# Kernel optimization log

Hardware: AMD Instinct MI355X
Metric: run time of the kernel (lower is better)

## Reference

```python
import jax, jax.numpy as jnp
import numpy as np

EMBED_DIM = 1024
NUM_HEADS = 16
HEAD_DIM = EMBED_DIM // NUM_HEADS
B, S = 4, 4096


def maxpool1d_2(x):
    # MaxPooling1D(pool_size=2, strides=2, padding='same'); seq len is even so no padding needed.
    n, l, d = x.shape
    return jnp.max(x.reshape(n, l // 2, 2, d), axis=2)


def setup_inputs() -> dict:
    key = jax.random.key(0)
    ks = jax.random.split(key, 5)
    scale = 1.0 / np.sqrt(EMBED_DIM)
    return {
        "x": jax.random.normal(ks[0], (B, S, EMBED_DIM), dtype=jnp.float32),
        "Wq": jax.random.normal(ks[1], (EMBED_DIM, EMBED_DIM), dtype=jnp.float32) * scale,
        "bq": jnp.zeros((EMBED_DIM,), dtype=jnp.float32),
        "Wk": jax.random.normal(ks[2], (EMBED_DIM, EMBED_DIM), dtype=jnp.float32) * scale,
        "bk": jnp.zeros((EMBED_DIM,), dtype=jnp.float32),
        "Wv": jax.random.normal(ks[3], (EMBED_DIM, EMBED_DIM), dtype=jnp.float32) * scale,
        "bv": jnp.zeros((EMBED_DIM,), dtype=jnp.float32),
        "Wo": jax.random.normal(ks[4], (EMBED_DIM, EMBED_DIM), dtype=jnp.float32) * scale,
        "bo": jnp.zeros((EMBED_DIM,), dtype=jnp.float32),
    }


def _separate_heads_pool(x, batch_size):
    # [B, S, E] -> [B, S, H, hd] -> [B, H, S, hd] -> [B*H, S, hd] -> pooled [B*H, S/2, hd]
    n, s, _ = x.shape
    x = x.reshape(batch_size, s, NUM_HEADS, HEAD_DIM).transpose(0, 2, 1, 3)
    x = x.reshape(batch_size * NUM_HEADS, s, HEAD_DIM)
    return maxpool1d_2(x)


def reference(x, Wq, bq, Wk, bk, Wv, bv, Wo, bo):
    batch_size = x.shape[0]
    q = x @ Wq + bq
    k = x @ Wk + bk
    v = x @ Wv + bv
    q = _separate_heads_pool(q, batch_size)  # [B*H, S/2, hd]
    k = _separate_heads_pool(k, batch_size)
    v = _separate_heads_pool(v, batch_size)
    score = jnp.einsum('nqd,nkd->nqk', q, k) / jnp.sqrt(jnp.float32(HEAD_DIM))
    weights = jax.nn.softmax(score, axis=-1)
    attn = jnp.einsum('nqk,nkd->nqd', weights, v)  # [B*H, S/2, hd]
    attn = maxpool1d_2(attn)  # [B*H, S/4, hd]
    # reshape back: (batch, -1, head_dim*num_heads). NOTE: original reshapes
    # [B*H, S/4, hd] directly to (B, -1, E) without transposing heads back,
    # so we replicate that exact layout.
    attn = attn.reshape(batch_size, -1, HEAD_DIM * NUM_HEADS)  # [B, S/4 (head-major mix), E]
    return attn @ Wo + bo
```

## Files before the change

### kernel.cpp

```cpp
#include <hip/hip_runtime.h>
#include <stdint.h>

typedef __attribute__((ext_vector_type(8))) __bf16 bf16x8;
typedef __attribute__((ext_vector_type(4))) float f32x4;
typedef __attribute__((ext_vector_type(8))) int i32x8;

#define DEV __device__ __forceinline__

DEV unsigned short f2bf(float f) {
  union { float f; uint32_t u; } v; v.f = f;
  return (unsigned short)((v.u + 0x7fffu + ((v.u >> 16) & 1u)) >> 16);
}

DEV uint32_t pk2bf(float lo, float hi) {
  union { float f; uint32_t u; } a, b;
  a.f = lo; b.f = hi;
  return __builtin_amdgcn_perm(b.u + 0x8000u, a.u + 0x8000u, 0x07060302u);
}

DEV void gld16(const void* g, void* l) {
  __builtin_amdgcn_global_load_lds(
      (const __attribute__((address_space(1))) uint32_t*)g,
      (__attribute__((address_space(3))) uint32_t*)l, 16, 0, 0);
}

union Frag8 { i32x8 v; uint4 q[2]; };

__global__ __launch_bounds__(256) void k_cvt_x(const float* __restrict__ x,
                                               uint8_t* __restrict__ x8) {
  size_t t = (size_t)blockIdx.x * 256 + threadIdx.x;
  const float4* xv = (const float4*)x;
  float4 a = xv[t * 2], b = xv[t * 2 + 1];
  int lo = 0, hi = 0;
  lo = __builtin_amdgcn_cvt_pk_fp8_f32(a.x, a.y, lo, false);
  lo = __builtin_amdgcn_cvt_pk_fp8_f32(a.z, a.w, lo, true);
  hi = __builtin_amdgcn_cvt_pk_fp8_f32(b.x, b.y, hi, false);
  hi = __builtin_amdgcn_cvt_pk_fp8_f32(b.z, b.w, hi, true);
  int2 pk; pk.x = lo; pk.y = hi;
  *(int2*)&x8[t * 8] = pk;
}

__global__ void k_cvt_w(const float* __restrict__ W0, const float* __restrict__ W1,
                        const float* __restrict__ W2, const float* __restrict__ W3,
                        uint8_t* __restrict__ W8, unsigned short* __restrict__ WoT) {
  const int z = blockIdx.z;
  const float* W = (z == 0) ? W0 : (z == 1) ? W1 : (z == 2) ? W2 : W3;
  __shared__ float tile[32][33];
  const int n0 = blockIdx.x * 32, k0 = blockIdx.y * 32;
  const int tx = threadIdx.x, ty = threadIdx.y;
  const int tid = ty * 32 + tx;
#pragma unroll
  for (int i = 0; i < 4; i++)
    tile[ty * 4 + i][tx] = W[(size_t)(k0 + ty * 4 + i) * 1024 + n0 + tx];
  __syncthreads();
  if (z < 3) {
    int nn = tid >> 3, kg = tid & 7;
    int w_ = 0;
    w_ = __builtin_amdgcn_cvt_pk_fp8_f32(32.f * tile[kg * 4 + 0][nn],
                                         32.f * tile[kg * 4 + 1][nn], w_, false);
    w_ = __builtin_amdgcn_cvt_pk_fp8_f32(32.f * tile[kg * 4 + 2][nn],
                                         32.f * tile[kg * 4 + 3][nn], w_, true);
    *(uint32_t*)&W8[(size_t)z * 1048576 + (size_t)(n0 + nn) * 1024 + k0 + kg * 4] =
        (uint32_t)w_;
  } else {
#pragma unroll
    for (int i = 0; i < 4; i++)
      WoT[(size_t)(n0 + ty * 4 + i) * 1024 + k0 + tx] = f2bf(tile[tx][ty * 4 + i]);
  }
}

__global__ __launch_bounds__(256) void k_gemm_qkv(
    const uint8_t* __restrict__ A, const uint8_t* __restrict__ W8,
    const float* __restrict__ bq, const float* __restrict__ bk,
    const float* __restrict__ bv,
    unsigned short* __restrict__ Qp, unsigned short* __restrict__ Kp,
    unsigned short* __restrict__ Vt) {
  const int tid = threadIdx.x;
  int flat = (blockIdx.z * 128 + blockIdx.y) * 8 + blockIdx.x;
  int swz = (flat & 7) * 384 + (flat >> 3);
  const int n0 = (swz & 7) * 128;
  const int m0 = ((swz >> 3) & 127) * 128;
  const int z = swz >> 10;
  const uint8_t* Bt = W8 + (size_t)z * 1048576;
  const float* bias = (z == 0) ? bq : (z == 1) ? bk : bv;

  __shared__ __align__(16) uint8_t lA[128 * 128];
  __shared__ __align__(16) uint8_t lB[128 * 128];

  const int lane = tid & 63, w = tid >> 6;
  const int wr = w >> 1, wc = w & 1;
  const int r = lane & 15, qd = lane >> 4;
  const int rl = lane >> 3, sg = lane & 7;

  f32x4 acc[4][4];
#pragma unroll
  for (int i = 0; i < 4; i++)
#pragma unroll
    for (int j = 0; j < 4; j++) acc[i][j] = (f32x4){0.f, 0.f, 0.f, 0.f};

  for (int k0 = 0; k0 < 1024; k0 += 128) {
    __syncthreads();
#pragma unroll
    for (int p = 0; p < 4; p++) {
      int row = (p * 4 + w) * 8 + rl;
      int g = sg ^ (row & 7);
      gld16(&A[(size_t)(m0 + row) * 1024 + k0 + g * 16], &lA[row * 128 + sg * 16]);
      gld16(&Bt[(size_t)(n0 + row) * 1024 + k0 + g * 16], &lB[row * 128 + sg * 16]);
    }
    __syncthreads();
    Frag8 bfr[4];
#pragma unroll
    for (int nt = 0; nt < 4; nt++) {
      int row = wc * 64 + nt * 16 + r;
      int g0 = (2 * qd) ^ (row & 7), g1 = (2 * qd + 1) ^ (row & 7);
      bfr[nt].q[0] = *(const uint4*)&lB[row * 128 + g0 * 16];
      bfr[nt].q[1] = *(const uint4*)&lB[row * 128 + g1 * 16];
    }
#pragma unroll
    for (int mt = 0; mt < 4; mt++) {
      int row = wr * 64 + mt * 16 + r;
      int g0 = (2 * qd) ^ (row & 7), g1 = (2 * qd + 1) ^ (row & 7);
      Frag8 af;
      af.q[0] = *(const uint4*)&lA[row * 128 + g0 * 16];
      af.q[1] = *(const uint4*)&lA[row * 128 + g1 * 16];
#pragma unroll
      for (int nt = 0; nt < 4; nt++)
        acc[mt][nt] = __builtin_amdgcn_mfma_scale_f32_16x16x128_f8f6f4(
            af.v, bfr[nt].v, acc[mt][nt], 0, 0, 0, 0x7f7f7f7f, 0, 0x7f7f7f7f);
    }
  }

  unsigned short* OP = (z == 0) ? Qp : Kp;
#pragma unroll
  for (int nt = 0; nt < 4; nt++) {
    int n = n0 + wc * 64 + nt * 16 + r;
    float bv_ = bias[n];
    int h = n >> 6, d = n & 63;
#pragma unroll
    for (int mt = 0; mt < 4; mt++) {
      int mg = m0 + wr * 64 + mt * 16 + qd * 4;
      int b = mg >> 12, s2 = (mg & 4095) >> 1;
      int bh = b * 16 + h;
      f32x4 a = acc[mt][nt];
      float v0 = fmaxf(a.x, a.y) * 0.03125f + bv_;
      float v1 = fmaxf(a.z, a.w) * 0.03125f + bv_;
      if (z == 2) {
        uint32_t pk = (uint32_t)f2bf(v0) | ((uint32_t)f2bf(v1) << 16);
        *(uint32_t*)&Vt[((size_t)bh * 64 + d) * 2048 + s2] = pk;
      } else {
        size_t base = ((size_t)bh * 2048 + s2) * 64 + d;
        OP[base] = f2bf(v0);
        OP[base + 64] = f2bf(v1);
      }
    }
  }
}

__global__ __launch_bounds__(256) void k_gemm_out(
    const unsigned short* __restrict__ A, const unsigned short* __restrict__ Bt,
    const float* __restrict__ bias, float* __restrict__ fout) {
  const int tid = threadIdx.x;
  int flat = blockIdx.y * 8 + blockIdx.x;
  int swz = (flat & 7) * 32 + (flat >> 3);
  const int n0 = (swz & 7) * 128, m0 = (swz >> 3) * 128;

  __shared__ __align__(16) unsigned short lA[128 * 64];
  __shared__ __align__(16) unsigned short lB[128 * 64];

  const int lane = tid & 63, w = tid >> 6;
  const int wr = w >> 1, wc = w & 1;
  const int r = lane & 15, qd = lane >> 4;
  const int srow = tid >> 3, sg = tid & 7;

  f32x4 acc[4][4];
#pragma unroll
  for (int i = 0; i < 4; i++)
#pragma unroll
    for (int j = 0; j < 4; j++) acc[i][j] = (f32x4){0.f, 0.f, 0.f, 0.f};

  for (int k0 = 0; k0 < 1024; k0 += 64) {
    __syncthreads();
#pragma unroll
    for (int p = 0; p < 4; p++) {
      int row = p * 32 + srow;
      int gs = sg ^ (row & 7);
      gld16(&A[(size_t)(m0 + row) * 1024 + k0 + gs * 8], &lA[row * 64 + sg * 8]);
      gld16(&Bt[(size_t)(n0 + row) * 1024 + k0 + gs * 8], &lB[row * 64 + sg * 8]);
    }
    __syncthreads();
#pragma unroll
    for (int kf = 0; kf < 2; kf++) {
      bf16x8 af[4], bfr[4];
#pragma unroll
      for (int mt = 0; mt < 4; mt++) {
        int row = wr * 64 + mt * 16 + r;
        int lg = (kf * 4 + qd) ^ (row & 7);
        af[mt] = *(const bf16x8*)&lA[row * 64 + lg * 8];
      }
#pragma unroll
      for (int nt = 0; nt < 4; nt++) {
        int row = wc * 64 + nt * 16 + r;
        int lg = (kf * 4 + qd) ^ (row & 7);
        bfr[nt] = *(const bf16x8*)&lB[row * 64 + lg * 8];
      }
#pragma unroll
      for (int mt = 0; mt < 4; mt++)
#pragma unroll
        for (int nt = 0; nt < 4; nt++)
          acc[mt][nt] = __builtin_amdgcn_mfma_f32_16x16x32_bf16(af[mt], bfr[nt],
                                                               acc[mt][nt], 0, 0, 0);
    }
  }

#pragma unroll
  for (int nt = 0; nt < 4; nt++) {
    int n = n0 + wc * 64 + nt * 16 + r;
    float bv = bias[n];
#pragma unroll
    for (int mt = 0; mt < 4; mt++) {
      int mg = m0 + wr * 64 + mt * 16 + qd * 4;
      f32x4 a = acc[mt][nt];
      fout[(size_t)(mg + 0) * 1024 + n] = a.x + bv;
      fout[(size_t)(mg + 1) * 1024 + n] = a.y + bv;
      fout[(size_t)(mg + 2) * 1024 + n] = a.z + bv;
      fout[(size_t)(mg + 3) * 1024 + n] = a.w + bv;
    }
  }
}

__global__ __launch_bounds__(256) void k_attn(const unsigned short* __restrict__ Qp,
                                              const unsigned short* __restrict__ Kp,
                                              const unsigned short* __restrict__ Vt,
                                              unsigned short* __restrict__ Am) {
  const int tid = threadIdx.x;
  int flat = blockIdx.y * 32 + blockIdx.x;
  int swz = (flat & 7) * 256 + (flat >> 3);
  const int qt = swz & 31, bh = swz >> 5;
  const int w = tid >> 6, lane = tid & 63;
  const int r = lane & 15, qd = lane >> 4;
  const int srow = tid >> 3, sg = tid & 7;

  __shared__ __align__(16) unsigned short lK[64 * 64];
  __shared__ __align__(16) unsigned short lV[64 * 64];
  __shared__ __align__(16) unsigned short lP[4][16 * 80];

  const int q0 = qt * 64;
  const int qrow = q0 + w * 16 + r;
  const size_t qbase = ((size_t)bh * 2048 + qrow) * 64;
  const bf16x8 bq0 = *(const bf16x8*)&Qp[qbase + qd * 8];
  const bf16x8 bq1 = *(const bf16x8*)&Qp[qbase + 32 + qd * 8];

  const unsigned short* Kg = Kp + (size_t)bh * 2048 * 64;
  const unsigned short* Vg = Vt + (size_t)bh * 64 * 2048;

  const float K2 = 0.125f * 1.44269504f;

  float lsum = 0.f;
  f32x4 accO[4];
#pragma unroll
  for (int i = 0; i < 4; i++) accO[i] = (f32x4){0.f, 0.f, 0.f, 0.f};

  char* lPw = (char*)&lP[w][0];

  for (int kb = 0; kb < 2048; kb += 64) {
    __syncthreads();
#pragma unroll
    for (int c = 0; c < 2; c++) {
      int row = c * 32 + srow;
      int gs = sg ^ (row & 7);
      gld16(&Kg[(size_t)(kb + row) * 64 + gs * 8], &lK[row * 64 + sg * 8]);
      gld16(&Vg[(size_t)row * 2048 + kb + gs * 8], &lV[row * 64 + sg * 8]);
    }
    __syncthreads();

    f32x4 s[4];
#pragma unroll
    for (int mt = 0; mt < 4; mt++) {
      int row = mt * 16 + r;
      int lg0 = qd ^ (row & 7), lg1 = (4 + qd) ^ (row & 7);
      bf16x8 ak0 = *(const bf16x8*)&lK[row * 64 + lg0 * 8];
      bf16x8 ak1 = *(const bf16x8*)&lK[row * 64 + lg1 * 8];
      s[mt] = (f32x4){0.f, 0.f, 0.f, 0.f};
      s[mt] = __builtin_amdgcn_mfma_f32_16x16x32_bf16(ak0, bq0, s[mt], 0, 0, 0);
      s[mt] = __builtin_amdgcn_mfma_f32_16x16x32_bf16(ak1, bq1, s[mt], 0, 0, 0);
    }

#pragma unroll
    for (int mt = 0; mt < 4; mt++) {
      float p0 = __builtin_amdgcn_exp2f(fmaf(s[mt][0], K2, -0.5f));
      float p1 = __builtin_amdgcn_exp2f(fmaf(s[mt][1], K2, -0.5f));
      float p2 = __builtin_amdgcn_exp2f(fmaf(s[mt][2], K2, -0.5f));
      float p3 = __builtin_amdgcn_exp2f(fmaf(s[mt][3], K2, -0.5f));
      lsum += (p0 + p1) + (p2 + p3);
      uint2 dw; dw.x = pk2bf(p0, p1); dw.y = pk2bf(p2, p3);
      int off = r * 160 + (((2 * mt + (qd >> 1)) ^ (r & 7)) << 4) + ((qd & 1) << 3);
      *(uint2*)(lPw + off) = dw;
    }

    bf16x8 ap0 = *(const bf16x8*)(lPw + r * 160 + ((qd ^ (r & 7)) << 4));
    bf16x8 ap1 = *(const bf16x8*)(lPw + r * 160 + (((4 + qd) ^ (r & 7)) << 4));

#pragma unroll
    for (int nt = 0; nt < 4; nt++) {
      int row = nt * 16 + r;
      int lg0 = qd ^ (row & 7), lg1 = (4 + qd) ^ (row & 7);
      bf16x8 bv0 = *(const bf16x8*)&lV[row * 64 + lg0 * 8];
      bf16x8 bv1 = *(const bf16x8*)&lV[row * 64 + lg1 * 8];
      accO[nt] = __builtin_amdgcn_mfma_f32_16x16x32_bf16(ap0, bv0, accO[nt], 0, 0, 0);
      accO[nt] = __builtin_amdgcn_mfma_f32_16x16x32_bf16(ap1, bv1, accO[nt], 0, 0, 0);
    }
  }

  lsum += __shfl_xor(lsum, 16, 64);
  lsum += __shfl_xor(lsum, 32, 64);
  float linv = 1.f / lsum;
  float inv[4];
#pragma unroll
  for (int g = 0; g < 4; g++) inv[g] = __shfl(linv, qd * 4 + g, 64);

#pragma unroll
  for (int nt = 0; nt < 4; nt++) {
    int d = nt * 16 + r;
    int s4 = (q0 + w * 16 + qd * 4) >> 1;
    float o0 = fmaxf(accO[nt][0] * inv[0], accO[nt][1] * inv[1]);
    float o1 = fmaxf(accO[nt][2] * inv[2], accO[nt][3] * inv[3]);
    size_t base = ((size_t)bh * 1024 + s4) * 64 + d;
    Am[base] = f2bf(o0);
    Am[base + 64] = f2bf(o1);
  }
}

extern "C" void kernel_launch(void* const* d_in, const int* in_sizes, int n_in,
                              void* d_out, int out_size, void* d_ws, size_t ws_size,
                              hipStream_t stream) {
  const float* x  = (const float*)d_in[0];
  const float* Wq = (const float*)d_in[1];
  const float* bq = (const float*)d_in[2];
  const float* Wk = (const float*)d_in[3];
  const float* bk = (const float*)d_in[4];
  const float* Wv = (const float*)d_in[5];
  const float* bv = (const float*)d_in[6];
  const float* Wo = (const float*)d_in[7];
  const float* bo = (const float*)d_in[8];
  float* out = (float*)d_out;

  uint8_t* ws = (uint8_t*)d_ws;
  uint8_t*        x8  = ws;
  uint8_t*        W8  = ws + 16777216;
  unsigned short* WoT = (unsigned short*)(ws + 19922944);
  unsigned short* Qp  = (unsigned short*)(ws + 22020096);
  unsigned short* Kp  = (unsigned short*)(ws + 38797312);
  unsigned short* Vt  = (unsigned short*)(ws + 55574528);
  unsigned short* Am  = (unsigned short*)(ws + 72351744);

  k_cvt_x<<<8192, 256, 0, stream>>>(x, x8);
  k_cvt_w<<<dim3(32, 32, 4), dim3(32, 8), 0, stream>>>(Wq, Wk, Wv, Wo, W8, WoT);
  k_gemm_qkv<<<dim3(8, 128, 3), 256, 0, stream>>>(x8, W8, bq, bk, bv, Qp, Kp, Vt);
  k_attn<<<dim3(32, 64), 256, 0, stream>>>(Qp, Kp, Vt, Am);
  k_gemm_out<<<dim3(8, 32), 256, 0, stream>>>(Am, WoT, bo, out);
}
```

Baseline: 360.0 us.

## Double-buffer LDS tiles in QKV GEMM, output GEMM, and attention kernels

Converts the shared-memory staging in all three kernels to two ping-pong buffers. The next K-slice (or K/V block) is issued via global_load_lds before the current buffer is consumed, and one barrier per iteration replaces two. The aim is to hide global-to-LDS load latency behind MFMA work. In exchange LDS use per block doubles, which may lower occupancy, and correctness depends on the compiler's waitcnt handling before the barrier.

```diff
diff --git a/kernel.cpp b/kernel.cpp
--- a/kernel.cpp
+++ b/kernel.cpp
@@ -84,8 +84,8 @@
   const uint8_t* Bt = W8 + (size_t)z * 1048576;
   const float* bias = (z == 0) ? bq : (z == 1) ? bk : bv;
 
-  __shared__ __align__(16) uint8_t lA[128 * 128];
-  __shared__ __align__(16) uint8_t lB[128 * 128];
+  __shared__ __align__(16) uint8_t lA[2][16384];
+  __shared__ __align__(16) uint8_t lB[2][16384];
 
   const int lane = tid & 63, w = tid >> 6;
   const int wr = w >> 1, wc = w & 1;
@@ -98,36 +98,56 @@
 #pragma unroll
     for (int j = 0; j < 4; j++) acc[i][j] = (f32x4){0.f, 0.f, 0.f, 0.f};
 
-  for (int k0 = 0; k0 < 1024; k0 += 128) {
-    __syncthreads();
-#pragma unroll
-    for (int p = 0; p < 4; p++) {
-      int row = (p * 4 + w) * 8 + rl;
-      int g = sg ^ (row & 7);
-      gld16(&A[(size_t)(m0 + row) * 1024 + k0 + g * 16], &lA[row * 128 + sg * 16]);
-      gld16(&Bt[(size_t)(n0 + row) * 1024 + k0 + g * 16], &lB[row * 128 + sg * 16]);
-    }
-    __syncthreads();
+  const uint8_t* gA[4]; const uint8_t* gB[4]; uint32_t lo[4];
+#pragma unroll
+  for (int p = 0; p < 4; p++) {
+    int row = (p * 4 + w) * 8 + rl;
+    int g = sg ^ (row & 7);
+    gA[p] = A + (size_t)(m0 + row) * 1024 + g * 16;
+    gB[p] = Bt + (size_t)(n0 + row) * 1024 + g * 16;
+    lo[p] = row * 128 + sg * 16;
+  }
+
+#pragma unroll
+  for (int p = 0; p < 4; p++) {
+    gld16(gA[p], &lA[0][lo[p]]);
+    gld16(gB[p], &lB[0][lo[p]]);
+  }
+  __syncthreads();
+
+#pragma unroll
+  for (int t = 0; t < 8; t++) {
+    const int cb = t & 1;
+    if (t < 7) {
+#pragma unroll
+      for (int p = 0; p < 4; p++) {
+        gld16(gA[p] + (t + 1) * 128, &lA[cb ^ 1][lo[p]]);
+        gld16(gB[p] + (t + 1) * 128, &lB[cb ^ 1][lo[p]]);
+      }
+    }
+    const uint8_t* lAc = lA[cb];
+    const uint8_t* lBc = lB[cb];
     Frag8 bfr[4];
 #pragma unroll
     for (int nt = 0; nt < 4; nt++) {
       int row = wc * 64 + nt * 16 + r;
       int g0 = (2 * qd) ^ (row & 7), g1 = (2 * qd + 1) ^ (row & 7);
-      bfr[nt].q[0] = *(const uint4*)&lB[row * 128 + g0 * 16];
-      bfr[nt].q[1] = *(const uint4*)&lB[row * 128 + g1 * 16];
+      bfr[nt].q[0] = *(const uint4*)&lBc[row * 128 + g0 * 16];
+      bfr[nt].q[1] = *(const uint4*)&lBc[row * 128 + g1 * 16];
     }
 #pragma unroll
     for (int mt = 0; mt < 4; mt++) {
       int row = wr * 64 + mt * 16 + r;
       int g0 = (2 * qd) ^ (row & 7), g1 = (2 * qd + 1) ^ (row & 7);
       Frag8 af;
-      af.q[0] = *(const uint4*)&lA[row * 128 + g0 * 16];
-      af.q[1] = *(const uint4*)&lA[row * 128 + g1 * 16];
+      af.q[0] = *(const uint4*)&lAc[row * 128 + g0 * 16];
+      af.q[1] = *(const uint4*)&lAc[row * 128 + g1 * 16];
 #pragma unroll
       for (int nt = 0; nt < 4; nt++)
         acc[mt][nt] = __builtin_amdgcn_mfma_scale_f32_16x16x128_f8f6f4(
             af.v, bfr[nt].v, acc[mt][nt], 0, 0, 0, 0x7f7f7f7f, 0, 0x7f7f7f7f);
     }
+    if (t < 7) __syncthreads();
   }
 
   unsigned short* OP = (z == 0) ? Qp : Kp;
@@ -164,8 +184,8 @@
   int swz = (flat & 7) * 32 + (flat >> 3);
   const int n0 = (swz & 7) * 128, m0 = (swz >> 3) * 128;
 
-  __shared__ __align__(16) unsigned short lA[128 * 64];
-  __shared__ __align__(16) unsigned short lB[128 * 64];
+  __shared__ __align__(16) unsigned short lA[2][8192];
+  __shared__ __align__(16) unsigned short lB[2][8192];
 
   const int lane = tid & 63, w = tid >> 6;
   const int wr = w >> 1, wc = w & 1;
@@ -178,16 +198,35 @@
 #pragma unroll
     for (int j = 0; j < 4; j++) acc[i][j] = (f32x4){0.f, 0.f, 0.f, 0.f};
 
-  for (int k0 = 0; k0 < 1024; k0 += 64) {
-    __syncthreads();
-#pragma unroll
-    for (int p = 0; p < 4; p++) {
-      int row = p * 32 + srow;
-      int gs = sg ^ (row & 7);
-      gld16(&A[(size_t)(m0 + row) * 1024 + k0 + gs * 8], &lA[row * 64 + sg * 8]);
-      gld16(&Bt[(size_t)(n0 + row) * 1024 + k0 + gs * 8], &lB[row * 64 + sg * 8]);
-    }
-    __syncthreads();
+  const unsigned short* gA[4]; const unsigned short* gB[4]; uint32_t lo[4];
+#pragma unroll
+  for (int p = 0; p < 4; p++) {
+    int row = p * 32 + srow;
+    int gs = sg ^ (row & 7);
+    gA[p] = A + (size_t)(m0 + row) * 1024 + gs * 8;
+    gB[p] = Bt + (size_t)(n0 + row) * 1024 + gs * 8;
+    lo[p] = row * 64 + sg * 8;
+  }
+
+#pragma unroll
+  for (int p = 0; p < 4; p++) {
+    gld16(gA[p], &lA[0][lo[p]]);
+    gld16(gB[p], &lB[0][lo[p]]);
+  }
+  __syncthreads();
+
+#pragma unroll
+  for (int t = 0; t < 16; t++) {
+    const int cb = t & 1;
+    if (t < 15) {
+#pragma unroll
+      for (int p = 0; p < 4; p++) {
+        gld16(gA[p] + (t + 1) * 64, &lA[cb ^ 1][lo[p]]);
+        gld16(gB[p] + (t + 1) * 64, &lB[cb ^ 1][lo[p]]);
+      }
+    }
+    const unsigned short* lAc = lA[cb];
+    const unsigned short* lBc = lB[cb];
 #pragma unroll
     for (int kf = 0; kf < 2; kf++) {
       bf16x8 af[4], bfr[4];
@@ -195,13 +234,13 @@
       for (int mt = 0; mt < 4; mt++) {
         int row = wr * 64 + mt * 16 + r;
         int lg = (kf * 4 + qd) ^ (row & 7);
-        af[mt] = *(const bf16x8*)&lA[row * 64 + lg * 8];
+        af[mt] = *(const bf16x8*)&lAc[row * 64 + lg * 8];
       }
 #pragma unroll
       for (int nt = 0; nt < 4; nt++) {
         int row = wc * 64 + nt * 16 + r;
         int lg = (kf * 4 + qd) ^ (row & 7);
-        bfr[nt] = *(const bf16x8*)&lB[row * 64 + lg * 8];
+        bfr[nt] = *(const bf16x8*)&lBc[row * 64 + lg * 8];
       }
 #pragma unroll
       for (int mt = 0; mt < 4; mt++)
@@ -210,6 +249,7 @@
           acc[mt][nt] = __builtin_amdgcn_mfma_f32_16x16x32_bf16(af[mt], bfr[nt],
                                                                acc[mt][nt], 0, 0, 0);
     }
+    if (t < 15) __syncthreads();
   }
 
 #pragma unroll
@@ -240,8 +280,8 @@
   const int r = lane & 15, qd = lane >> 4;
   const int srow = tid >> 3, sg = tid & 7;
 
-  __shared__ __align__(16) unsigned short lK[64 * 64];
-  __shared__ __align__(16) unsigned short lV[64 * 64];
+  __shared__ __align__(16) unsigned short lK[2][4096];
+  __shared__ __align__(16) unsigned short lV[2][4096];
   __shared__ __align__(16) unsigned short lP[4][16 * 80];
 
   const int q0 = qt * 64;
@@ -262,52 +302,76 @@
 
   char* lPw = (char*)&lP[w][0];
 
-  for (int kb = 0; kb < 2048; kb += 64) {
-    __syncthreads();
-#pragma unroll
-    for (int c = 0; c < 2; c++) {
-      int row = c * 32 + srow;
-      int gs = sg ^ (row & 7);
-      gld16(&Kg[(size_t)(kb + row) * 64 + gs * 8], &lK[row * 64 + sg * 8]);
-      gld16(&Vg[(size_t)row * 2048 + kb + gs * 8], &lV[row * 64 + sg * 8]);
-    }
-    __syncthreads();
-
-    f32x4 s[4];
-#pragma unroll
-    for (int mt = 0; mt < 4; mt++) {
-      int row = mt * 16 + r;
-      int lg0 = qd ^ (row & 7), lg1 = (4 + qd) ^ (row & 7);
-      bf16x8 ak0 = *(const bf16x8*)&lK[row * 64 + lg0 * 8];
-      bf16x8 ak1 = *(const bf16x8*)&lK[row * 64 + lg1 * 8];
-      s[mt] = (f32x4){0.f, 0.f, 0.f, 0.f};
-      s[mt] = __builtin_amdgcn_mfma_f32_16x16x32_bf16(ak0, bq0, s[mt], 0, 0, 0);
-      s[mt] = __builtin_amdgcn_mfma_f32_16x16x32_bf16(ak1, bq1, s[mt], 0, 0, 0);
-    }
-
-#pragma unroll
-    for (int mt = 0; mt < 4; mt++) {
-      float p0 = __builtin_amdgcn_exp2f(fmaf(s[mt][0], K2, -0.5f));
-      float p1 = __builtin_amdgcn_exp2f(fmaf(s[mt][1], K2, -0.5f));
-      float p2 = __builtin_amdgcn_exp2f(fmaf(s[mt][2], K2, -0.5f));
-      float p3 = __builtin_amdgcn_exp2f(fmaf(s[mt][3], K2, -0.5f));
-      lsum += (p0 + p1) + (p2 + p3);
-      uint2 dw; dw.x = pk2bf(p0, p1); dw.y = pk2bf(p2, p3);
-      int off = r * 160 + (((2 * mt + (qd >> 1)) ^ (r & 7)) << 4) + ((qd & 1) << 3);
-      *(uint2*)(lPw + off) = dw;
-    }
-
-    bf16x8 ap0 = *(const bf16x8*)(lPw + r * 160 + ((qd ^ (r & 7)) << 4));
-    bf16x8 ap1 = *(const bf16x8*)(lPw + r * 160 + (((4 + qd) ^ (r & 7)) << 4));
-
-#pragma unroll
-    for (int nt = 0; nt < 4; nt++) {
-      int row = nt * 16 + r;
-      int lg0 = qd ^ (row & 7), lg1 = (4 + qd) ^ (row & 7);
-      bf16x8 bv0 = *(const bf16x8*)&lV[row * 64 + lg0 * 8];
-      bf16x8 bv1 = *(const bf16x8*)&lV[row * 64 + lg1 * 8];
-      accO[nt] = __builtin_amdgcn_mfma_f32_16x16x32_bf16(ap0, bv0, accO[nt], 0, 0, 0);
-      accO[nt] = __builtin_amdgcn_mfma_f32_16x16x32_bf16(ap1, bv1, accO[nt], 0, 0, 0);
+  const unsigned short* gK[2]; const unsigned short* gV[2]; uint32_t loKV[2];
+#pragma unroll
+  for (int c = 0; c < 2; c++) {
+    int row = c * 32 + srow;
+    int gs = sg ^ (row & 7);
+    gK[c] = Kg + (size_t)row * 64 + gs * 8;
+    gV[c] = Vg + (size_t)row * 2048 + gs * 8;
+    loKV[c] = row * 64 + sg * 8;
+  }
+
+#pragma unroll
+  for (int c = 0; c < 2; c++) {
+    gld16(gK[c], &lK[0][loKV[c]]);
+    gld16(gV[c], &lV[0][loKV[c]]);
+  }
+  __syncthreads();
+
+  for (int kb2 = 0; kb2 < 2048; kb2 += 128) {
+#pragma unroll
+    for (int ph = 0; ph < 2; ph++) {
+      const int cb = ph;
+      const int kn = kb2 + ph * 64 + 64;
+      if (kn < 2048) {
+#pragma unroll
+        for (int c = 0; c < 2; c++) {
+          gld16(gK[c] + (size_t)kn * 64, &lK[cb ^ 1][loKV[c]]);
+          gld16(gV[c] + kn, &lV[cb ^ 1][loKV[c]]);
+        }
+      }
+
+      const unsigned short* lKc = lK[cb];
+      const unsigned short* lVc = lV[cb];
+
+      f32x4 s[4];
+#pragma unroll
+      for (int mt = 0; mt < 4; mt++) {
+        int row = mt * 16 + r;
+        int lg0 = qd ^ (row & 7), lg1 = (4 + qd) ^ (row & 7);
+        bf16x8 ak0 = *(const bf16x8*)&lKc[row * 64 + lg0 * 8];
+        bf16x8 ak1 = *(const bf16x8*)&lKc[row * 64 + lg1 * 8];
+        s[mt] = (f32x4){0.f, 0.f, 0.f, 0.f};
+        s[mt] = __builtin_amdgcn_mfma_f32_16x16x32_bf16(ak0, bq0, s[mt], 0, 0, 0);
+        s[mt] = __builtin_amdgcn_mfma_f32_16x16x32_bf16(ak1, bq1, s[mt], 0, 0, 0);
+      }
+
+#pragma unroll
+      for (int mt = 0; mt < 4; mt++) {
+        float p0 = __builtin_amdgcn_exp2f(fmaf(s[mt][0], K2, -0.5f));
+        float p1 = __builtin_amdgcn_exp2f(fmaf(s[mt][1], K2, -0.5f));
+        float p2 = __builtin_amdgcn_exp2f(fmaf(s[mt][2], K2, -0.5f));
+        float p3 = __builtin_amdgcn_exp2f(fmaf(s[mt][3], K2, -0.5f));
+        lsum += (p0 + p1) + (p2 + p3);
+        uint2 dw; dw.x = pk2bf(p0, p1); dw.y = pk2bf(p2, p3);
+        int off = r * 160 + (((2 * mt + (qd >> 1)) ^ (r & 7)) << 4) + ((qd & 1) << 3);
+        *(uint2*)(lPw + off) = dw;
+      }
+
+      bf16x8 ap0 = *(const bf16x8*)(lPw + r * 160 + ((qd ^ (r & 7)) << 4));
+      bf16x8 ap1 = *(const bf16x8*)(lPw + r * 160 + (((4 + qd) ^ (r & 7)) << 4));
+
+#pragma unroll
+      for (int nt = 0; nt < 4; nt++) {
+        int row = nt * 16 + r;
+        int lg0 = qd ^ (row & 7), lg1 = (4 + qd) ^ (row & 7);
+        bf16x8 bv0 = *(const bf16x8*)&lVc[row * 64 + lg0 * 8];
+        bf16x8 bv1 = *(const bf16x8*)&lVc[row * 64 + lg1 * 8];
+        accO[nt] = __builtin_amdgcn_mfma_f32_16x16x32_bf16(ap0, bv0, accO[nt], 0, 0, 0);
+        accO[nt] = __builtin_amdgcn_mfma_f32_16x16x32_bf16(ap1, bv1, accO[nt], 0, 0, 0);
+      }
+      __syncthreads();
     }
   }
 
```

Result: faster. 348.0 us (-3.3%).
